# Kernel tuning notes

Measured on AMD Instinct MI355X. Metric: run time of the kernel, lower is better.

The kernel has to match this reference:

```python
import jax, jax.numpy as jnp
from jax import lax
import numpy as np

DIM = 512
HEADS = 8


def setup_inputs() -> dict:
    key = jax.random.key(0)
    k1, k2, k3, k4, k5 = jax.random.split(key, 5)
    B, C, H, W = 2, DIM, 64, 64
    x = jax.random.normal(k1, (B, C, H, W), dtype=jnp.float32)
    # depthwise 3x3 conv (groups=C, bias=False): torch OIHW with O=C, I=1
    dw_w = jax.random.normal(k2, (C, 1, 3, 3), dtype=jnp.float32) * (1.0 / 3.0)
    # 1x1 conv C -> 3C (bias=False)
    qkv_w = jax.random.normal(k3, (3 * C, C, 1, 1), dtype=jnp.float32) * (C ** -0.5)
    # 1x1 proj conv C -> C with bias
    proj_w = jax.random.normal(k4, (C, C, 1, 1), dtype=jnp.float32) * (C ** -0.5)
    proj_b = jax.random.normal(k5, (C,), dtype=jnp.float32) * 0.01
    return {"x": x, "dw_w": dw_w, "qkv_w": qkv_w, "proj_w": proj_w, "proj_b": proj_b}


def reference(x, dw_w, qkv_w, proj_w, proj_b):
    B, C, H, W = x.shape
    heads = HEADS
    dh = C // heads
    scale = dh ** -0.5
    N = H * W
    # depthwise 3x3, padding=1
    y = lax.conv_general_dilated(
        x, dw_w, window_strides=(1, 1), padding=((1, 1), (1, 1)),
        dimension_numbers=("NCHW", "OIHW", "NCHW"), feature_group_count=C)
    # 1x1 conv as matmul over channels -> (B, 3C, H, W)
    qkv = jnp.einsum("bchw,oc->bohw", y, qkv_w[:, :, 0, 0])
    # (B, 3, heads, dh, N) -> q,k,v each (B, heads, N, dh)
    qkv = qkv.reshape(B, 3, heads, dh, N).transpose(1, 0, 2, 4, 3)
    q, k, v = qkv[0], qkv[1], qkv[2]
    attn = jax.nn.softmax(jnp.einsum("bhnd,bhmd->bhnm", q, k) * scale, axis=-1)
    o = jnp.einsum("bhnm,bhmd->bhnd", attn, v)          # (B, heads, N, dh)
    o = o.transpose(0, 1, 3, 2).reshape(B, C, H, W)      # matches torch transpose(2,3).reshape
    out = jnp.einsum("bchw,oc->bohw", o, proj_w[:, :, 0, 0]) + proj_b[None, :, None, None]
    return out
```

## Files before the change

kernel.cpp:

```cpp
#include <hip/hip_runtime.h>
#include <hip/hip_bf16.h>

typedef __bf16 bf16_t;
typedef __bf16 bf16x4 __attribute__((ext_vector_type(4)));
typedef __bf16 bf16x8 __attribute__((ext_vector_type(8)));
typedef float f32x4 __attribute__((ext_vector_type(4)));
typedef float f32x8 __attribute__((ext_vector_type(8)));

#define MFMA16(a, b, c) __builtin_amdgcn_mfma_f32_16x16x32_bf16((a), (b), (c), 0, 0, 0)

#if __has_builtin(__builtin_amdgcn_exp2f)
#define EXP2(x) __builtin_amdgcn_exp2f(x)
#else
#define EXP2(x) exp2f(x)
#endif

#define AS1(p) ((const __attribute__((address_space(1))) void*)(p))
#define AS3(p) ((__attribute__((address_space(3))) void*)(p))

#define NPIX 4096
#define CDIM 512
#define QSCALE 0.1803368801111744f

__device__ __forceinline__ bool detect_f32(const void* p) {
  const unsigned short* u = (const unsigned short*)p;
  int lane = threadIdx.x & 63;
  int f = 0;
#pragma unroll
  for (int j = 0; j < 4; ++j) {
    int e = (u[lane * 4 + j] >> 7) & 0xFF;
    f |= (e >= 138) ? 1 : 0;
  }
  return __ballot(f) != 0ull;
}

__global__ __launch_bounds__(256) void dwconv_kernel(
    const void* __restrict__ x_, const void* __restrict__ dww_,
    bf16_t* __restrict__ yt) {
  __shared__ bf16_t xs[64 * 194];
  __shared__ float wsh[64 * 9];
  const bool f32m = detect_f32(x_);
  int bidx = blockIdx.x;
  int c0 = (bidx & 7) << 6;
  int h = (bidx >> 3) & 63;
  int b = bidx >> 9;
  int tid = threadIdx.x;

  for (int i = tid; i < 576; i += 256)
    wsh[i] = f32m ? ((const float*)dww_)[c0 * 9 + i]
                  : (float)((const bf16_t*)dww_)[c0 * 9 + i];

  const size_t xoff = ((size_t)b * CDIM + c0) * NPIX;
#pragma unroll
  for (int r = 0; r < 3; ++r) {
    int hh = h + r - 1;
    bool ok = (unsigned)hh < 64u;
#pragma unroll
    for (int it = 0; it < 2; ++it) {
      int idx2 = tid + it * 256;
      int c = idx2 >> 3, ch = idx2 & 7;
      bf16x8 v = {};
      if (ok) {
        size_t gi = xoff + (size_t)c * NPIX + (size_t)hh * 64 + ch * 8;
        if (f32m) {
          const float* p = (const float*)x_ + gi;
          float4 t0 = *(const float4*)p;
          float4 t1 = *(const float4*)(p + 4);
          v[0] = (bf16_t)t0.x; v[1] = (bf16_t)t0.y;
          v[2] = (bf16_t)t0.z; v[3] = (bf16_t)t0.w;
          v[4] = (bf16_t)t1.x; v[5] = (bf16_t)t1.y;
          v[6] = (bf16_t)t1.z; v[7] = (bf16_t)t1.w;
        } else {
          v = *(const bf16x8*)((const bf16_t*)x_ + gi);
        }
      }
      union { bf16x8 v8; unsigned u[4]; } uu;
      uu.v8 = v;
      unsigned* dst = (unsigned*)&xs[c * 194 + r * 64 + ch * 8];
      dst[0] = uu.u[0]; dst[1] = uu.u[1]; dst[2] = uu.u[2]; dst[3] = uu.u[3];
    }
  }
  __syncthreads();

  int c = tid & 63;
  int wb = tid >> 6;
  float wreg[9];
#pragma unroll
  for (int j = 0; j < 9; ++j) wreg[j] = wsh[c * 9 + j];
  const bf16_t* xrow = &xs[c * 194];
  bf16_t* ybase = yt + ((size_t)b * NPIX + h * 64) * CDIM + c0 + c;
#pragma unroll
  for (int jj = 0; jj < 16; ++jj) {
    int w = wb + 4 * jj;
    float acc = 0.f;
#pragma unroll
    for (int r = 0; r < 3; ++r) {
      float xm = (w > 0) ? (float)xrow[r * 64 + w - 1] : 0.f;
      float xc = (float)xrow[r * 64 + w];
      float xp = (w < 63) ? (float)xrow[r * 64 + w + 1] : 0.f;
      acc += xm * wreg[3 * r] + xc * wreg[3 * r + 1] + xp * wreg[3 * r + 2];
    }
    ybase[(size_t)w * CDIM] = (bf16_t)acc;
  }
}

__global__ __launch_bounds__(256) void gemm_kernel(
    const void* __restrict__ A_, const bf16_t* __restrict__ Bt,
    void* __restrict__ o0, bf16_t* __restrict__ o1, bf16_t* __restrict__ o2,
    const void* __restrict__ bias_, int mode,
    const bf16_t* __restrict__ O2p, const float* __restrict__ lsb) {
  const int K = 512;
  __shared__ bf16_t as[128 * 32];
  __shared__ bf16_t bs[128 * 32];
  const bool f32m = detect_f32(A_);
  int z = blockIdx.z;
  const bf16_t* Bz = Bt + (size_t)z * NPIX * K;
  int m0 = blockIdx.x * 128;
  int n0 = blockIdx.y * 128;
  int tid = threadIdx.x;
  int lane = tid & 63;
  int wv = tid >> 6;
  int wm = wv >> 1, wn = wv & 1;
  int col = lane & 15, quad = lane >> 4;

  f32x4 acc[4][4] = {};
  for (int ko = 0; ko < K; ko += 32) {
    if (!f32m) {
#pragma unroll
      for (int j = 0; j < 2; ++j) {
        int i = tid + j * 256;
        int row = i >> 2, kc = (i & 3) << 3;
        __builtin_amdgcn_global_load_lds(
            AS1(&((const bf16_t*)A_)[(size_t)(m0 + row) * K + ko + kc]),
            AS3(&as[(wv * 64 + j * 256) * 8]), 16, 0, 0);
      }
    } else {
#pragma unroll
      for (int j = 0; j < 2; ++j) {
        int i = tid + j * 256;
        int row = i >> 2, kc = (i & 3) << 3;
        const float* p = &((const float*)A_)[(size_t)(m0 + row) * K + ko + kc];
        float4 t0 = *(const float4*)p;
        float4 t1 = *(const float4*)(p + 4);
        bf16x8 av;
        av[0] = (bf16_t)t0.x; av[1] = (bf16_t)t0.y;
        av[2] = (bf16_t)t0.z; av[3] = (bf16_t)t0.w;
        av[4] = (bf16_t)t1.x; av[5] = (bf16_t)t1.y;
        av[6] = (bf16_t)t1.z; av[7] = (bf16_t)t1.w;
        *(bf16x8*)&as[row * 32 + kc] = av;
      }
    }
    if (mode != 2) {
#pragma unroll
      for (int j = 0; j < 2; ++j) {
        int i = tid + j * 256;
        int row = i >> 2, kc = (i & 3) << 3;
        __builtin_amdgcn_global_load_lds(
            AS1(&Bz[(size_t)(n0 + row) * K + ko + kc]),
            AS3(&bs[(wv * 64 + j * 256) * 8]), 16, 0, 0);
      }
    } else {
#pragma unroll
      for (int j = 0; j < 2; ++j) {
        int i = tid + j * 256;
        int row = i >> 2, kc = (i & 3) << 3;
        int hz = ko >> 6;
        size_t qi = (size_t)(z * 8 + hz) * NPIX + n0 + row;
        float invl = 1.f / (lsb[qi] + lsb[qi + 16 * (size_t)NPIX]);
        int d = (ko & 63) + kc;
        bf16x8 p1 = *(const bf16x8*)&Bt[qi * 64 + d];
        bf16x8 p2 = *(const bf16x8*)&O2p[qi * 64 + d];
        f32x8 f;
#pragma unroll
        for (int e = 0; e < 8; ++e)
          f[e] = ((float)p1[e] + (float)p2[e]) * invl;
        *(bf16x8*)&bs[row * 32 + kc] = __builtin_convertvector(f, bf16x8);
      }
    }
    __syncthreads();

    bf16x8 af[4], bfr[4];
#pragma unroll
    for (int f = 0; f < 4; ++f) {
      af[f] = *(const bf16x8*)&as[(wm * 64 + f * 16 + col) * 32 + quad * 8];
      bfr[f] = *(const bf16x8*)&bs[(wn * 64 + f * 16 + col) * 32 + quad * 8];
    }
#pragma unroll
    for (int fm = 0; fm < 4; ++fm)
#pragma unroll
      for (int fn = 0; fn < 4; ++fn)
        acc[fm][fn] = MFMA16(af[fm], bfr[fn], acc[fm][fn]);
    __syncthreads();
  }

  if (mode == 0) {
    int t = m0 >> 9;
    float scale = (t == 0) ? QSCALE : 1.0f;
    bf16_t* q0 = (bf16_t*)o0;
#pragma unroll
    for (int fm = 0; fm < 4; ++fm) {
      int mloc = m0 + wm * 64 + fm * 16 + quad * 4;
      int hh = (mloc & 511) >> 6;
      int d = mloc & 63;
#pragma unroll
      for (int fn = 0; fn < 4; ++fn) {
        int n = n0 + wn * 64 + fn * 16 + col;
        if (t < 2) {
          bf16_t* dst = ((t == 0) ? q0 : o1) +
                        ((size_t)z * 8 + hh) * ((size_t)NPIX * 64) +
                        (size_t)n * 64 + d;
          union {
            ushort4 u;
            bf16_t hv[4];
          } pk;
#pragma unroll
          for (int r = 0; r < 4; ++r) pk.hv[r] = (bf16_t)(acc[fm][fn][r] * scale);
          *(ushort4*)dst = pk.u;
        } else {
          bf16_t* vb = o2 + ((size_t)z * 8 + hh) * ((size_t)NPIX * 64);
#pragma unroll
          for (int r = 0; r < 4; ++r)
            vb[(size_t)(d + r) * NPIX + n] = (bf16_t)acc[fm][fn][r];
        }
      }
    }
  } else {
#pragma unroll
    for (int fm = 0; fm < 4; ++fm) {
      int mloc = m0 + wm * 64 + fm * 16 + quad * 4;
#pragma unroll
      for (int r = 0; r < 4; ++r) {
        float bv = f32m ? ((const float*)bias_)[mloc + r]
                        : (float)((const bf16_t*)bias_)[mloc + r];
#pragma unroll
        for (int fn = 0; fn < 4; ++fn) {
          int n = n0 + wn * 64 + fn * 16 + col;
          size_t oi = (size_t)z * CDIM * NPIX + (size_t)(mloc + r) * NPIX + n;
          float val = acc[fm][fn][r] + bv;
          if (f32m)
            ((float*)o0)[oi] = val;
          else
            ((bf16_t*)o0)[oi] = (bf16_t)val;
        }
      }
    }
  }
}

template <int MODE>
__global__ __launch_bounds__(256, 2) void attn_kernel(
    const bf16_t* __restrict__ q, const bf16_t* __restrict__ k,
    const bf16_t* __restrict__ vt, bf16_t* __restrict__ po,
    size_t posz, float* __restrict__ lsum) {
  __shared__ bf16_t ks[2 * 64 * 72];
  __shared__ bf16_t vs[2 * 64 * 72];
  int qt = blockIdx.x & 15;
  int bh = (blockIdx.x >> 4) & 15;
  int kh = (MODE == 2) ? (blockIdx.x >> 8) : 0;
  const int kspan = (MODE == 2) ? 32 : 64;
  int kstart = kh * kspan;
  int kend = kstart + kspan;
  int tid = threadIdx.x;
  int lane = tid & 63, wv = tid >> 6;
  int col = lane & 15, quad = lane >> 4;
  const bf16_t* qb = q + (size_t)bh * NPIX * 64;
  const bf16_t* kb = k + (size_t)bh * NPIX * 64;
  const bf16_t* vb = vt + (size_t)bh * NPIX * 64;

  bf16x8 qfrag[4][2];
  int qrow0 = qt * 256 + wv * 64;
#pragma unroll
  for (int sub = 0; sub < 4; ++sub)
#pragma unroll
    for (int kk = 0; kk < 2; ++kk)
      qfrag[sub][kk] = *(const bf16x8*)&qb[(size_t)(qrow0 + sub * 16 + col) * 64 +
                                           kk * 32 + quad * 8];

  int trow = tid >> 2, t4 = tid & 3;
  bf16x8 kA0, kA1, vA0, vA1, kB0, kB1, vB0, vB1;
  auto loadKV = [&](int kc, bf16x8& k0, bf16x8& k1, bf16x8& v0, bf16x8& v1) {
    const bf16_t* kgr = &kb[(size_t)(kc * 64 + trow) * 64 + t4 * 16];
    const bf16_t* vgr = &vb[(size_t)trow * NPIX + kc * 64 + t4 * 16];
    k0 = *(const bf16x8*)kgr;
    k1 = *(const bf16x8*)(kgr + 8);
    v0 = *(const bf16x8*)vgr;
    v1 = *(const bf16x8*)(vgr + 8);
  };
  loadKV(kstart, kA0, kA1, vA0, vA1);
  loadKV(kstart + 1, kB0, kB1, vB0, vB1);

  int vbase = trow * 72 + (t4 >> 1) * 32 + (t4 & 1) * 4;

  f32x4 oacc[4][4] = {};
  float lsv[4] = {0.f, 0.f, 0.f, 0.f};

  for (int kc = kstart; kc < kend; ++kc) {
    bf16_t* ksb = &ks[(kc & 1) * 4608];
    bf16_t* vsb = &vs[(kc & 1) * 4608];
    *(bf16x8*)&ksb[trow * 72 + t4 * 16] = kA0;
    *(bf16x8*)&ksb[trow * 72 + t4 * 16 + 8] = kA1;
    {
      union { bf16x8 v; bf16x4 h[2]; } u0, u1;
      u0.v = vA0; u1.v = vA1;
      *(bf16x4*)&vsb[vbase] = u0.h[0];
      *(bf16x4*)&vsb[vbase + 8] = u0.h[1];
      *(bf16x4*)&vsb[vbase + 16] = u1.h[0];
      *(bf16x4*)&vsb[vbase + 24] = u1.h[1];
    }
    __syncthreads();

    kA0 = kB0; kA1 = kB1; vA0 = vB0; vA1 = vB1;
    {
      int kcn = kc + 2;
      if (kcn >= kend) kcn = kstart;
      loadKV(kcn, kB0, kB1, vB0, vB1);
    }

    bf16x8 kf[4][2];
#pragma unroll
    for (int nt = 0; nt < 4; ++nt)
#pragma unroll
      for (int kk = 0; kk < 2; ++kk)
        kf[nt][kk] =
            *(const bf16x8*)&ksb[(nt * 16 + col) * 72 + kk * 32 + quad * 8];
    bf16x8 vf[4][2];
#pragma unroll
    for (int dt = 0; dt < 4; ++dt)
#pragma unroll
      for (int t = 0; t < 2; ++t)
        vf[dt][t] =
            *(const bf16x8*)&vsb[(dt * 16 + col) * 72 + t * 32 + quad * 8];

#pragma unroll
    for (int sub = 0; sub < 4; ++sub) {
      f32x4 sv[4];
#pragma unroll
      for (int nt = 0; nt < 4; ++nt) {
        f32x4 s = {};
        s = MFMA16(kf[nt][0], qfrag[sub][0], s);
        s = MFMA16(kf[nt][1], qfrag[sub][1], s);
        sv[nt] = s;
      }
      bf16x8 pb[2];
      float ls = 0.f;
#pragma unroll
      for (int t = 0; t < 2; ++t) {
        f32x8 pe;
#pragma unroll
        for (int half = 0; half < 2; ++half)
#pragma unroll
          for (int r = 0; r < 4; ++r)
            pe[half * 4 + r] = EXP2(sv[2 * t + half][r]);
        float s0 = pe[0] + pe[1], s1 = pe[2] + pe[3];
        float s2 = pe[4] + pe[5], s3 = pe[6] + pe[7];
        ls += (s0 + s1) + (s2 + s3);
        pb[t] = __builtin_convertvector(pe, bf16x8);
      }
      lsv[sub] += ls;
#pragma unroll
      for (int dt = 0; dt < 4; ++dt) {
        oacc[sub][dt] = MFMA16(vf[dt][0], pb[0], oacc[sub][dt]);
        oacc[sub][dt] = MFMA16(vf[dt][1], pb[1], oacc[sub][dt]);
      }
    }
  }

#pragma unroll
  for (int sub = 0; sub < 4; ++sub) {
    lsv[sub] += __shfl_xor(lsv[sub], 16);
    lsv[sub] += __shfl_xor(lsv[sub], 32);
  }

  if (MODE == 0) {
    int b = bh >> 3, hh = bh & 7;
#pragma unroll
    for (int sub = 0; sub < 4; ++sub) {
      float inv = 1.f / lsv[sub];
      int qrow = qrow0 + sub * 16 + col;
      bf16_t* ob = po + ((size_t)b * NPIX + qrow) * CDIM + hh * 64 + quad * 4;
#pragma unroll
      for (int dt = 0; dt < 4; ++dt) {
        union {
          ushort4 u;
          bf16_t hv[4];
        } pk;
#pragma unroll
        for (int r = 0; r < 4; ++r)
          pk.hv[r] = (bf16_t)(oacc[sub][dt][r] * inv);
        *(ushort4*)(ob + dt * 16) = pk.u;
      }
    }
  } else {
    bf16_t* pbase = po + (size_t)kh * posz;
#pragma unroll
    for (int sub = 0; sub < 4; ++sub) {
      int qrow = qrow0 + sub * 16 + col;
      bf16_t* op = pbase + ((size_t)bh * NPIX + qrow) * 64 + quad * 4;
#pragma unroll
      for (int dt = 0; dt < 4; ++dt) {
        union {
          ushort4 u;
          bf16_t hv[4];
        } pk;
#pragma unroll
        for (int r = 0; r < 4; ++r) pk.hv[r] = (bf16_t)oacc[sub][dt][r];
        *(ushort4*)(op + dt * 16) = pk.u;
      }
    }
    if (quad == 0) {
      float* lbase = lsum + (size_t)(kh * 16 + bh) * NPIX;
#pragma unroll
      for (int sub = 0; sub < 4; ++sub)
        lbase[qrow0 + sub * 16 + col] = lsv[sub];
    }
  }
}

extern "C" void kernel_launch(void* const* d_in, const int* in_sizes, int n_in,
                              void* d_out, int out_size, void* d_ws,
                              size_t ws_size, hipStream_t stream) {
  const void* x = d_in[0];
  const void* dww = d_in[1];
  const void* qkvw = d_in[2];
  const void* projw = d_in[3];
  const void* projb = d_in[4];

  bf16_t* ws = (bf16_t*)d_ws;
  const size_t SZ = (size_t)2 * NPIX * CDIM;
  bf16_t* yt = ws;
  bf16_t* qa = ws + SZ;
  bf16_t* ka = ws + 2 * SZ;
  bf16_t* va = ws + 3 * SZ;

  const size_t need2 =
      5 * SZ * sizeof(bf16_t) + 2 * 16 * (size_t)NPIX * sizeof(float);

  dwconv_kernel<<<1024, 256, 0, stream>>>(x, dww, yt);
  gemm_kernel<<<dim3(12, 32, 2), 256, 0, stream>>>(
      qkvw, yt, qa, ka, va, nullptr, 0, nullptr, nullptr);

  if (ws_size >= need2) {
    bf16_t* O1 = yt;
    bf16_t* O2 = ws + 4 * SZ;
    float* ls2 = (float*)(ws + 5 * SZ);
    attn_kernel<2><<<512, 256, 0, stream>>>(qa, ka, va, O1,
                                            (size_t)(O2 - O1), ls2);
    gemm_kernel<<<dim3(4, 32, 2), 256, 0, stream>>>(
        projw, O1, d_out, nullptr, nullptr, projb, 2, O2, ls2);
  } else {
    attn_kernel<0><<<256, 256, 0, stream>>>(qa, ka, va, yt, 0, nullptr);
    gemm_kernel<<<dim3(4, 32, 2), 256, 0, stream>>>(
        projw, yt, d_out, nullptr, nullptr, projb, 1, nullptr, nullptr);
  }
}
```

Baseline: 208.3 us.

## Split attention keys four ways and generalize partial-sum merge in projection GEMM

Attention now splits the key range into four chunks instead of two, launching 1024 blocks with launch bounds raised to 4 blocks per CU, and writes four partial outputs and row sums to a larger workspace. The projection GEMM merges a variable number of partials using a stride parameter. It also adds s_setprio around the MFMA sections to favor matrix issue. The goal is more parallelism and better latency hiding in attention, at the cost of extra partial-output traffic and merge work, and a new 4-way path that runs only when the workspace is large enough.

```diff
diff --git a/kernel.cpp b/kernel.cpp
--- a/kernel.cpp
+++ b/kernel.cpp
@@ -107,8 +107,8 @@
 __global__ __launch_bounds__(256) void gemm_kernel(
     const void* __restrict__ A_, const bf16_t* __restrict__ Bt,
     void* __restrict__ o0, bf16_t* __restrict__ o1, bf16_t* __restrict__ o2,
-    const void* __restrict__ bias_, int mode,
-    const bf16_t* __restrict__ O2p, const float* __restrict__ lsb) {
+    const void* __restrict__ bias_, int mode, size_t pstride,
+    const float* __restrict__ lsb) {
   const int K = 512;
   __shared__ bf16_t as[128 * 32];
   __shared__ bf16_t bs[128 * 32];
@@ -150,7 +150,7 @@
         *(bf16x8*)&as[row * 32 + kc] = av;
       }
     }
-    if (mode != 2) {
+    if (mode < 2) {
 #pragma unroll
       for (int j = 0; j < 2; ++j) {
         int i = tid + j * 256;
@@ -166,14 +166,19 @@
         int row = i >> 2, kc = (i & 3) << 3;
         int hz = ko >> 6;
         size_t qi = (size_t)(z * 8 + hz) * NPIX + n0 + row;
-        float invl = 1.f / (lsb[qi] + lsb[qi + 16 * (size_t)NPIX]);
+        float lacc = 0.f;
+        for (int s = 0; s < mode; ++s)
+          lacc += lsb[qi + (size_t)s * 16 * NPIX];
+        float invl = 1.f / lacc;
         int d = (ko & 63) + kc;
-        bf16x8 p1 = *(const bf16x8*)&Bt[qi * 64 + d];
-        bf16x8 p2 = *(const bf16x8*)&O2p[qi * 64 + d];
-        f32x8 f;
-#pragma unroll
-        for (int e = 0; e < 8; ++e)
-          f[e] = ((float)p1[e] + (float)p2[e]) * invl;
+        f32x8 f = {};
+        for (int s = 0; s < mode; ++s) {
+          bf16x8 p = *(const bf16x8*)&Bt[(size_t)s * pstride + qi * 64 + d];
+#pragma unroll
+          for (int e = 0; e < 8; ++e) f[e] += (float)p[e];
+        }
+#pragma unroll
+        for (int e = 0; e < 8; ++e) f[e] *= invl;
         *(bf16x8*)&bs[row * 32 + kc] = __builtin_convertvector(f, bf16x8);
       }
     }
@@ -248,7 +253,7 @@
 }
 
 template <int MODE>
-__global__ __launch_bounds__(256, 2) void attn_kernel(
+__global__ __launch_bounds__(256, 4) void attn_kernel(
     const bf16_t* __restrict__ q, const bf16_t* __restrict__ k,
     const bf16_t* __restrict__ vt, bf16_t* __restrict__ po,
     size_t posz, float* __restrict__ lsum) {
@@ -256,8 +261,8 @@
   __shared__ bf16_t vs[2 * 64 * 72];
   int qt = blockIdx.x & 15;
   int bh = (blockIdx.x >> 4) & 15;
-  int kh = (MODE == 2) ? (blockIdx.x >> 8) : 0;
-  const int kspan = (MODE == 2) ? 32 : 64;
+  int kh = (MODE >= 2) ? (blockIdx.x >> 8) : 0;
+  const int kspan = (MODE >= 2) ? (64 / MODE) : 64;
   int kstart = kh * kspan;
   int kend = kstart + kspan;
   int tid = threadIdx.x;
@@ -334,6 +339,7 @@
 #pragma unroll
     for (int sub = 0; sub < 4; ++sub) {
       f32x4 sv[4];
+      __builtin_amdgcn_s_setprio(1);
 #pragma unroll
       for (int nt = 0; nt < 4; ++nt) {
         f32x4 s = {};
@@ -341,6 +347,7 @@
         s = MFMA16(kf[nt][1], qfrag[sub][1], s);
         sv[nt] = s;
       }
+      __builtin_amdgcn_s_setprio(0);
       bf16x8 pb[2];
       float ls = 0.f;
 #pragma unroll
@@ -357,11 +364,13 @@
         pb[t] = __builtin_convertvector(pe, bf16x8);
       }
       lsv[sub] += ls;
+      __builtin_amdgcn_s_setprio(1);
 #pragma unroll
       for (int dt = 0; dt < 4; ++dt) {
         oacc[sub][dt] = MFMA16(vf[dt][0], pb[0], oacc[sub][dt]);
         oacc[sub][dt] = MFMA16(vf[dt][1], pb[1], oacc[sub][dt]);
       }
+      __builtin_amdgcn_s_setprio(0);
     }
   }
 
@@ -432,24 +441,30 @@
   bf16_t* ka = ws + 2 * SZ;
   bf16_t* va = ws + 3 * SZ;
 
+  const size_t need4 =
+      8 * SZ * sizeof(bf16_t) + 4 * 16 * (size_t)NPIX * sizeof(float);
   const size_t need2 =
       5 * SZ * sizeof(bf16_t) + 2 * 16 * (size_t)NPIX * sizeof(float);
 
   dwconv_kernel<<<1024, 256, 0, stream>>>(x, dww, yt);
   gemm_kernel<<<dim3(12, 32, 2), 256, 0, stream>>>(
-      qkvw, yt, qa, ka, va, nullptr, 0, nullptr, nullptr);
-
-  if (ws_size >= need2) {
+      qkvw, yt, qa, ka, va, nullptr, 0, 0, nullptr);
+
+  if (ws_size >= need4) {
+    bf16_t* O1 = ws + 4 * SZ;
+    float* ls4 = (float*)(ws + 8 * SZ);
+    attn_kernel<4><<<1024, 256, 0, stream>>>(qa, ka, va, O1, SZ, ls4);
+    gemm_kernel<<<dim3(4, 32, 2), 256, 0, stream>>>(
+        projw, O1, d_out, nullptr, nullptr, projb, 4, SZ, ls4);
+  } else if (ws_size >= need2) {
     bf16_t* O1 = yt;
-    bf16_t* O2 = ws + 4 * SZ;
     float* ls2 = (float*)(ws + 5 * SZ);
-    attn_kernel<2><<<512, 256, 0, stream>>>(qa, ka, va, O1,
-                                            (size_t)(O2 - O1), ls2);
+    attn_kernel<2><<<512, 256, 0, stream>>>(qa, ka, va, O1, 4 * SZ, ls2);
     gemm_kernel<<<dim3(4, 32, 2), 256, 0, stream>>>(
-        projw, O1, d_out, nullptr, nullptr, projb, 2, O2, ls2);
+        projw, O1, d_out, nullptr, nullptr, projb, 2, 4 * SZ, ls2);
   } else {
     attn_kernel<0><<<256, 256, 0, stream>>>(qa, ka, va, yt, 0, nullptr);
     gemm_kernel<<<dim3(4, 32, 2), 256, 0, stream>>>(
-        projw, yt, d_out, nullptr, nullptr, projb, 1, nullptr, nullptr);
+        projw, yt, d_out, nullptr, nullptr, projb, 1, 0, nullptr);
   }
 }
```

Result: slower. 770.5 us (+269.9%).
